# Optimization experiments

Hardware: AMD Instinct MI355X
Metric: run time of the kernel (lower is better)

## Reference

```python
import jax, jax.numpy as jnp
import numpy as np

B, S, E, H = 4, 2048, 1024, 16
HD = E // H  # per-head dim = 64


def setup_inputs() -> dict:
    key = jax.random.key(0)
    ks = jax.random.split(key, 12)
    scale = 1.0 / np.sqrt(E)
    inp = {
        "q": jax.random.normal(ks[0], (B, S, E), jnp.float32),
        "k": jax.random.normal(ks[1], (B, S, E), jnp.float32),
        "v": jax.random.normal(ks[2], (B, S, E), jnp.float32),
        # causal mask: True = masked out (matches torch masked_fill_ semantics)
        "mask": jnp.triu(jnp.ones((S, S), jnp.bool_), k=1)[None, None, :, :],
        "Wq": jax.random.normal(ks[3], (E, E), jnp.float32) * scale,
        "bq": jnp.zeros((E,), jnp.float32),
        "Wk": jax.random.normal(ks[4], (E, E), jnp.float32) * scale,
        "bk": jnp.zeros((E,), jnp.float32),
        "Wv": jax.random.normal(ks[5], (E, E), jnp.float32) * scale,
        "bv": jnp.zeros((E,), jnp.float32),
        "Wo": jax.random.normal(ks[6], (E, E), jnp.float32) * scale,
        "bo": jnp.zeros((E,), jnp.float32),
    }
    return inp


def reference(q, k, v, mask, Wq, bq, Wk, bk, Wv, bv, Wo, bo):
    # QKV projections (nn.Linear: x @ W.T + b)
    query = q @ Wq.T + bq
    key_ = k @ Wk.T + bk
    value = v @ Wv.T + bv
    # split heads: [B, S, E] -> [B, H, S, HD]
    mq = query.reshape(B, S, H, HD).transpose(0, 2, 1, 3)
    mk = key_.reshape(B, S, H, HD).transpose(0, 2, 1, 3)
    mv = value.reshape(B, S, H, HD).transpose(0, 2, 1, 3)
    # scaled dot-product attention with explicit score matrix [B, H, S, S]
    scores = jnp.einsum("bhqd,bhkd->bhqk", mq, mk) / jnp.sqrt(jnp.float32(HD))
    scores = jnp.where(mask, -jnp.inf, scores)
    probs = jax.nn.softmax(scores, axis=-1)
    ctx = jnp.einsum("bhqk,bhkd->bhqd", probs, mv)
    # merge heads and output projection
    ctx = ctx.transpose(0, 2, 1, 3).reshape(B, S, E)
    return ctx @ Wo.T + bo
```

## Files before the change

### kernel.cpp

```cpp
#include <hip/hip_runtime.h>
#include <hip/hip_bf16.h>
#include <math.h>

#define B_ 4
#define S_ 2048
#define E_ 1024
#define H_ 16
#define HD_ 64
#define NEG_ (-1e30f)
#define SC2_ 0.18033688f
#define EXP2(x) __builtin_amdgcn_exp2f(x)

typedef __bf16 bf16x8 __attribute__((ext_vector_type(8)));
typedef __bf16 bf16x4 __attribute__((ext_vector_type(4)));
typedef float f32x4 __attribute__((ext_vector_type(4)));

#define MFMA(a, b, c) __builtin_amdgcn_mfma_f32_16x16x32_bf16((a), (b), (c), 0, 0, 0)

#define GLDS16(gp, lp)                                                        \
  __builtin_amdgcn_global_load_lds(                                           \
      (const __attribute__((address_space(1))) void*)(gp),                    \
      (__attribute__((address_space(3))) void*)(lp), 16, 0, 0)

__device__ __forceinline__ bf16x8 cvt8(const float4 a, const float4 b) {
  bf16x8 r;
  r[0] = (__bf16)a.x; r[1] = (__bf16)a.y; r[2] = (__bf16)a.z; r[3] = (__bf16)a.w;
  r[4] = (__bf16)b.x; r[5] = (__bf16)b.y; r[6] = (__bf16)b.z; r[7] = (__bf16)b.w;
  return r;
}

__device__ __forceinline__ f32x4 vmax4(f32x4 a, f32x4 b) {
  f32x4 r;
  r[0] = fmaxf(a[0], b[0]); r[1] = fmaxf(a[1], b[1]);
  r[2] = fmaxf(a[2], b[2]); r[3] = fmaxf(a[3], b[3]);
  return r;
}

__global__ __launch_bounds__(256)
void cvt_all_kernel(const float* __restrict__ q, const float* __restrict__ k,
                    const float* __restrict__ v,
                    const float* __restrict__ wq, const float* __restrict__ wk,
                    const float* __restrict__ wv, const float* __restrict__ wo,
                    __bf16* __restrict__ q16, __bf16* __restrict__ k16,
                    __bf16* __restrict__ v16,
                    __bf16* __restrict__ wqb, __bf16* __restrict__ wkb,
                    __bf16* __restrict__ wvb, __bf16* __restrict__ wob)
{
  const int bx = blockIdx.x;
  const float* src;
  __bf16* dst;
  size_t off;
  if (bx < 12288) {
    const int z = bx >> 12, r = bx & 4095;
    src = (z == 0) ? q : (z == 1) ? k : v;
    dst = (z == 0) ? q16 : (z == 1) ? k16 : v16;
    off = (size_t)r * 2048 + threadIdx.x * 8;
  } else {
    const int z = (bx - 12288) >> 9, r = (bx - 12288) & 511;
    src = (z == 0) ? wq : (z == 1) ? wk : (z == 2) ? wv : wo;
    dst = (z == 0) ? wqb : (z == 1) ? wkb : (z == 2) ? wvb : wob;
    off = (size_t)r * 2048 + threadIdx.x * 8;
  }
  const float4 a = *(const float4*)&src[off];
  const float4 b = *(const float4*)&src[off + 4];
  *(bf16x8*)&dst[off] = cvt8(a, b);
}

__global__ __launch_bounds__(256)
void cvt_w_kernel(const float* __restrict__ wq, const float* __restrict__ wk,
                  const float* __restrict__ wv, const float* __restrict__ wo,
                  __bf16* __restrict__ wqb, __bf16* __restrict__ wkb,
                  __bf16* __restrict__ wvb, __bf16* __restrict__ wob)
{
  const int y = blockIdx.y;
  const float* src = (y == 0) ? wq : (y == 1) ? wk : (y == 2) ? wv : wo;
  __bf16* dst      = (y == 0) ? wqb: (y == 1) ? wkb: (y == 2) ? wvb: wob;
  const size_t i = ((size_t)blockIdx.x * 256 + threadIdx.x) * 8;
  const float4 a = *(const float4*)&src[i];
  const float4 b = *(const float4*)&src[i + 4];
  *(bf16x8*)&dst[i] = cvt8(a, b);
}

__global__ __launch_bounds__(256)
void cvt_in_kernel(const float* __restrict__ src, __bf16* __restrict__ dst)
{
  const size_t i = ((size_t)blockIdx.x * 256 + threadIdx.x) * 8;
  const float4 a = *(const float4*)&src[i];
  const float4 b = *(const float4*)&src[i + 4];
  *(bf16x8*)&dst[i] = cvt8(a, b);
}

__global__ __launch_bounds__(256, 3)
void qkv_gemm(const __bf16* __restrict__ Aq, const __bf16* __restrict__ Ak,
              const __bf16* __restrict__ Av,
              const __bf16* __restrict__ Wqb, const __bf16* __restrict__ Wkb,
              const __bf16* __restrict__ Wvb,
              const float* __restrict__ bq, const float* __restrict__ bk,
              const float* __restrict__ bv,
              __bf16* __restrict__ Qo, __bf16* __restrict__ Ko,
              __bf16* __restrict__ Vo, int zbase)
{
  __shared__ __align__(16) __bf16 sAB[2][128 * 64];
  __bf16* const sA = sAB[0];
  __bf16* const sB = sAB[1];
  const int z = (int)blockIdx.z + zbase;
  const __bf16* A   = (z == 0) ? Aq  : (z == 1) ? Ak  : Av;
  const __bf16* W   = (z == 0) ? Wqb : (z == 1) ? Wkb : Wvb;
  const float* bias = (z == 0) ? bq  : (z == 1) ? bk  : bv;

  const int t = threadIdx.x;
  const int lane = t & 63, ln = lane & 15, qd = lane >> 4;
  const int l7 = ln & 7;
  const int wv_ = t >> 6, wm = (wv_ >> 1) * 64, wn = (wv_ & 1) * 64;
  const int m0 = ((int)blockIdx.x * 8 + ((int)blockIdx.y >> 3)) * 128;
  const int n0 = ((int)blockIdx.y & 7) * 128;

  f32x4 acc[4][4] = {};
  for (int kk = 0; kk < E_; kk += 64) {
    __syncthreads();
    for (int p = 0; p < 4; ++p) {
      const int c = t + 256 * p;
      const int row = c >> 3, kc = c & 7;
      const int gcol = ((kc ^ (row & 7)) * 8);
      GLDS16(A + (size_t)(m0 + row) * E_ + kk + gcol, sA + c * 8);
      GLDS16(W + (size_t)(n0 + row) * E_ + kk + gcol, sB + c * 8);
    }
    __syncthreads();
    for (int kb2 = 0; kb2 < 2; ++kb2) {
      const int sw = ((kb2 * 4 + qd) ^ l7) * 8;
      bf16x8 af[4], bf_[4];
      for (int i = 0; i < 4; ++i)
        af[i]  = *(const bf16x8*)&sA[(wm + i * 16 + ln) * 64 + sw];
      for (int j = 0; j < 4; ++j)
        bf_[j] = *(const bf16x8*)&sB[(wn + j * 16 + ln) * 64 + sw];
      for (int i = 0; i < 4; ++i)
        for (int j = 0; j < 4; ++j)
          acc[i][j] = MFMA(af[i], bf_[j], acc[i][j]);
    }
  }

  if (z < 2) {
    __bf16* outp = (z == 0) ? Qo : Ko;
    for (int j = 0; j < 4; ++j) {
      const int n = n0 + wn + j * 16 + ln;
      const float bb = bias[n];
      const int hh = n >> 6, d = n & 63;
      for (int i = 0; i < 4; ++i) {
        for (int r2 = 0; r2 < 4; ++r2) {
          const int m = m0 + wm + i * 16 + qd * 4 + r2;
          const int b = m >> 11, s2 = m & 2047;
          float val = acc[i][j][r2] + bb;
          if (z == 0) val *= SC2_;
          outp[((size_t)(b * H_ + hh) * S_ + s2) * HD_ + d] = (__bf16)val;
        }
      }
    }
  } else {
    __syncthreads();
    __bf16* const sT = &sAB[0][0];
    for (int j = 0; j < 4; ++j) {
      const int nl = wn + j * 16 + ln;
      const float bb = bias[n0 + nl];
      const int rsw = (nl & 7) << 3;
      for (int i = 0; i < 4; ++i)
        for (int r2 = 0; r2 < 4; ++r2) {
          const int ml = wm + i * 16 + qd * 4 + r2;
          sT[nl * 128 + (ml ^ rsw)] = (__bf16)(acc[i][j][r2] + bb);
        }
    }
    __syncthreads();
    const int r = t >> 1, half = t & 1;
    const int n = n0 + r, hh = n >> 6, d = n & 63;
    const int b = m0 >> 11, s0 = m0 & 2047;
    __bf16* dstp = Vo + ((size_t)(b * H_ + hh) * HD_ + d) * S_ + s0 + half * 64;
    const int rsw = (r & 7) << 3;
    for (int c8 = 0; c8 < 8; ++c8) {
      const int mc = half * 64 + c8 * 8;
      bf16x8 vv = *(const bf16x8*)&sT[r * 128 + (mc ^ rsw)];
      *(bf16x8*)&dstp[c8 * 8] = vv;
    }
  }
}

__global__ __launch_bounds__(256, 3)
void attn_kernel(const __bf16* __restrict__ Qg, const __bf16* __restrict__ Kg,
                 const __bf16* __restrict__ Vg, __bf16* __restrict__ Og)
{
  const int slice = blockIdx.x;
  const int h = slice & 15, b = slice >> 4;
  const int qx = 31 - (int)blockIdx.y;
  const int t = threadIdx.x;
  const int wq = t >> 6;
  const int lane = t & 63;
  const int ln = lane & 15, qd = lane >> 4;
  const int l7 = ln & 7;
  const int q0 = qx * 64;
  const size_t bh = (size_t)(b * H_ + h);

  __shared__ __align__(16) __bf16 sK[128 * 64];
  __shared__ __align__(16) __bf16 sVt[64 * 128];
  __shared__ __align__(16) __bf16 sP[64 * 136];

  bf16x8 aq[2];
  {
    const __bf16* qrowp = Qg + (bh * S_ + q0 + wq * 16 + ln) * HD_;
    aq[0] = *(const bf16x8*)&qrowp[qd * 8];
    aq[1] = *(const bf16x8*)&qrowp[32 + qd * 8];
  }

  const int myq = q0 + wq * 16 + ln;

  f32x4 o[4] = {};
  float m_prev = NEG_, l_run = 0.f;

  const int ktmax = (q0 + 63) >> 7;
  for (int kt = 0; kt <= ktmax; ++kt) {
    const int k0 = kt * 128;
    __syncthreads();
    {
      const __bf16* kbase = Kg + (bh * S_ + k0) * HD_;
      const __bf16* vbase = Vg + bh * HD_ * S_ + k0;
      for (int p = 0; p < 4; ++p) {
        const int c = t + 256 * p;
        const int kr = c >> 3, kkc = c & 7;
        GLDS16(kbase + (size_t)kr * HD_ + ((kkc ^ (kr & 7)) * 8), sK + c * 8);
        const int vr = c >> 4, vkc = c & 15;
        GLDS16(vbase + (size_t)vr * S_ + ((vkc ^ (vr & 15)) * 8), sVt + c * 8);
      }
    }
    __syncthreads();

    f32x4 sc[8] = {};
    for (int kb2 = 0; kb2 < 2; ++kb2) {
      const int sw = ((kb2 * 4 + qd) ^ l7) * 8;
      for (int nt = 0; nt < 8; ++nt) {
        bf16x8 ak8 = *(const bf16x8*)&sK[(nt * 16 + ln) * 64 + sw];
        sc[nt] = MFMA(ak8, aq[kb2], sc[nt]);
      }
    }

    if (k0 + 127 > q0) {
      const int kb = k0 + qd * 4 - myq;
      for (int nt = 0; nt < 8; ++nt)
        for (int r2 = 0; r2 < 4; ++r2)
          if (kb + nt * 16 + r2 > 0) sc[nt][r2] = NEG_;
    }

    f32x4 t0 = vmax4(vmax4(sc[0], sc[1]), vmax4(sc[2], sc[3]));
    f32x4 t1 = vmax4(vmax4(sc[4], sc[5]), vmax4(sc[6], sc[7]));
    f32x4 t2 = vmax4(t0, t1);
    float mloc = fmaxf(fmaxf(t2[0], t2[1]), fmaxf(t2[2], t2[3]));
    mloc = fmaxf(mloc, __shfl_xor(mloc, 16, 64));
    mloc = fmaxf(mloc, __shfl_xor(mloc, 32, 64));

    if (!__all(mloc - m_prev <= 8.0f)) {
      const float m_new = fmaxf(m_prev, mloc);
      const float alpha = EXP2(m_prev - m_new);
      m_prev = m_new;
      l_run *= alpha;
      float af[4];
      for (int r2 = 0; r2 < 4; ++r2)
        af[r2] = __shfl(alpha, qd * 4 + r2, 64);
      for (int dt = 0; dt < 4; ++dt)
        for (int r2 = 0; r2 < 4; ++r2)
          o[dt][r2] *= af[r2];
    }

    float rsum = 0.f;
    {
      const int pb = (wq * 16 + ln) * 136 + qd * 4;
      for (int nt = 0; nt < 8; ++nt) {
        const float p0 = EXP2(sc[nt][0] - m_prev);
        const float p1 = EXP2(sc[nt][1] - m_prev);
        const float p2 = EXP2(sc[nt][2] - m_prev);
        const float p3 = EXP2(sc[nt][3] - m_prev);
        rsum += (p0 + p1) + (p2 + p3);
        bf16x4 pk;
        pk[0] = (__bf16)p0; pk[1] = (__bf16)p1;
        pk[2] = (__bf16)p2; pk[3] = (__bf16)p3;
        *(bf16x4*)&sP[pb + nt * 16] = pk;
      }
    }
    rsum += __shfl_xor(rsum, 16, 64);
    rsum += __shfl_xor(rsum, 32, 64);
    l_run += rsum;

    for (int ks = 0; ks < 4; ++ks) {
      bf16x8 ap = *(const bf16x8*)&sP[(wq * 16 + ln) * 136 + ks * 32 + qd * 8];
      const int swv = ((ks * 4 + qd) ^ ln) * 8;
      for (int dt = 0; dt < 4; ++dt) {
        bf16x8 bv8 = *(const bf16x8*)&sVt[(dt * 16 + ln) * 128 + swv];
        o[dt] = MFMA(ap, bv8, o[dt]);
      }
    }
  }

  const float linv = 1.0f / l_run;
  float inv[4];
  for (int r2 = 0; r2 < 4; ++r2)
    inv[r2] = __shfl(linv, qd * 4 + r2, 64);
  for (int r2 = 0; r2 < 4; ++r2) {
    const int qrow = q0 + wq * 16 + qd * 4 + r2;
    for (int dt = 0; dt < 4; ++dt) {
      const int d = dt * 16 + ln;
      Og[((size_t)(b * S_ + qrow)) * E_ + h * HD_ + d] = (__bf16)(o[dt][r2] * inv[r2]);
    }
  }
}

__global__ __launch_bounds__(256, 3)
void out_gemm(const __bf16* __restrict__ A, const __bf16* __restrict__ W,
              const float* __restrict__ bias, float* __restrict__ out)
{
  __shared__ __align__(16) __bf16 sA[128 * 64];
  __shared__ __align__(16) __bf16 sB[128 * 64];
  const int t = threadIdx.x;
  const int lane = t & 63, ln = lane & 15, qd = lane >> 4;
  const int l7 = ln & 7;
  const int wv_ = t >> 6, wm = (wv_ >> 1) * 64, wn = (wv_ & 1) * 64;
  const int m0 = blockIdx.y * 128, n0 = blockIdx.x * 128;

  f32x4 acc[4][4] = {};
  for (int kk = 0; kk < E_; kk += 64) {
    __syncthreads();
    for (int p = 0; p < 4; ++p) {
      const int c = t + 256 * p;
      const int row = c >> 3, kc = c & 7;
      const int gcol = ((kc ^ (row & 7)) * 8);
      GLDS16(A + (size_t)(m0 + row) * E_ + kk + gcol, sA + c * 8);
      GLDS16(W + (size_t)(n0 + row) * E_ + kk + gcol, sB + c * 8);
    }
    __syncthreads();
    for (int kb2 = 0; kb2 < 2; ++kb2) {
      const int sw = ((kb2 * 4 + qd) ^ l7) * 8;
      bf16x8 af[4], bf_[4];
      for (int i = 0; i < 4; ++i)
        af[i]  = *(const bf16x8*)&sA[(wm + i * 16 + ln) * 64 + sw];
      for (int j = 0; j < 4; ++j)
        bf_[j] = *(const bf16x8*)&sB[(wn + j * 16 + ln) * 64 + sw];
      for (int i = 0; i < 4; ++i)
        for (int j = 0; j < 4; ++j)
          acc[i][j] = MFMA(af[i], bf_[j], acc[i][j]);
    }
  }

  for (int j = 0; j < 4; ++j) {
    const int n = n0 + wn + j * 16 + ln;
    const float bb = bias[n];
    for (int i = 0; i < 4; ++i)
      for (int r2 = 0; r2 < 4; ++r2) {
        const int m = m0 + wm + i * 16 + qd * 4 + r2;
        out[(size_t)m * E_ + n] = acc[i][j][r2] + bb;
      }
  }
}

extern "C" void kernel_launch(void* const* d_in, const int* in_sizes, int n_in,
                              void* d_out, int out_size, void* d_ws, size_t ws_size,
                              hipStream_t stream)
{
  const float* q  = (const float*)d_in[0];
  const float* k  = (const float*)d_in[1];
  const float* v  = (const float*)d_in[2];
  const float* Wq = (const float*)d_in[4];
  const float* bq = (const float*)d_in[5];
  const float* Wk = (const float*)d_in[6];
  const float* bk = (const float*)d_in[7];
  const float* Wv = (const float*)d_in[8];
  const float* bv = (const float*)d_in[9];
  const float* Wo = (const float*)d_in[10];
  const float* bo = (const float*)d_in[11];
  float* out = (float*)d_out;

  const size_t NE = (size_t)B_ * S_ * E_;
  const size_t NW = (size_t)E_ * E_;
  __bf16* Wqb = (__bf16*)d_ws;
  __bf16* Wkb = Wqb + NW;
  __bf16* Wvb = Wkb + NW;
  __bf16* Wob = Wvb + NW;
  __bf16* Qb  = Wob + NW;
  __bf16* Kb  = Qb + NE;
  __bf16* Vb  = Kb + NE;

  dim3 blk(256);
  const size_t need_fat = (4 * NW + 6 * NE) * sizeof(__bf16);
  if (ws_size >= need_fat) {
    __bf16* q16 = Vb + NE;
    __bf16* k16 = q16 + NE;
    __bf16* v16 = k16 + NE;
    __bf16* Cb  = q16;
    cvt_all_kernel<<<dim3(14336), blk, 0, stream>>>(q, k, v, Wq, Wk, Wv, Wo,
                                                    q16, k16, v16,
                                                    Wqb, Wkb, Wvb, Wob);
    qkv_gemm<<<dim3(8, 64, 3), blk, 0, stream>>>(q16, k16, v16,
                                                 Wqb, Wkb, Wvb,
                                                 bq, bk, bv, Qb, Kb, Vb, 0);
    attn_kernel<<<dim3(64, 32), blk, 0, stream>>>(Qb, Kb, Vb, Cb);
    out_gemm<<<dim3(8, 64), blk, 0, stream>>>(Cb, Wob, bo, out);
  } else {
    cvt_w_kernel<<<dim3(512, 4), blk, 0, stream>>>(Wq, Wk, Wv, Wo,
                                                   Wqb, Wkb, Wvb, Wob);
    __bf16* X16 = Vb + NE;
    __bf16* Cb  = X16;
    const float* srcs[3] = {q, k, v};
    for (int z = 0; z < 3; ++z) {
      cvt_in_kernel<<<dim3(4096), blk, 0, stream>>>(srcs[z], X16);
      qkv_gemm<<<dim3(8, 64, 1), blk, 0, stream>>>(X16, X16, X16,
                                                   Wqb, Wkb, Wvb,
                                                   bq, bk, bv, Qb, Kb, Vb, z);
    }
    attn_kernel<<<dim3(64, 32), blk, 0, stream>>>(Qb, Kb, Vb, Cb);
    out_gemm<<<dim3(8, 64), blk, 0, stream>>>(Cb, Wob, bo, out);
  }
}
```

Baseline: 325.9 us.

## Switch attention kernel to 32x32 MFMA with 128-row query tiles

The attention kernel now gives each wave 32 query rows and uses 32x32x16 bf16 MFMA instead of 16x16x32, with the query tile per block grown to 128 rows and the key tile shrunk to 64. Each K/V tile loaded into LDS is reused by more query rows, fewer blocks are launched, and waves whose rows are fully masked skip the tile. The costs are a larger register footprint for the 16-element accumulators, fewer blocks in the grid, and a different causal-masking and LDS swizzle layout.

```diff
diff --git a/kernel.cpp b/kernel.cpp
--- a/kernel.cpp
+++ b/kernel.cpp
@@ -14,8 +14,10 @@
 typedef __bf16 bf16x8 __attribute__((ext_vector_type(8)));
 typedef __bf16 bf16x4 __attribute__((ext_vector_type(4)));
 typedef float f32x4 __attribute__((ext_vector_type(4)));
+typedef float f32x16 __attribute__((ext_vector_type(16)));
 
 #define MFMA(a, b, c) __builtin_amdgcn_mfma_f32_16x16x32_bf16((a), (b), (c), 0, 0, 0)
+#define MFMA32(a, b, c) __builtin_amdgcn_mfma_f32_32x32x16_bf16((a), (b), (c), 0, 0, 0)
 
 #define GLDS16(gp, lp)                                                        \
   __builtin_amdgcn_global_load_lds(                                           \
@@ -26,13 +28,6 @@
   bf16x8 r;
   r[0] = (__bf16)a.x; r[1] = (__bf16)a.y; r[2] = (__bf16)a.z; r[3] = (__bf16)a.w;
   r[4] = (__bf16)b.x; r[5] = (__bf16)b.y; r[6] = (__bf16)b.z; r[7] = (__bf16)b.w;
-  return r;
-}
-
-__device__ __forceinline__ f32x4 vmax4(f32x4 a, f32x4 b) {
-  f32x4 r;
-  r[0] = fmaxf(a[0], b[0]); r[1] = fmaxf(a[1], b[1]);
-  r[2] = fmaxf(a[2], b[2]); r[3] = fmaxf(a[3], b[3]);
   return r;
 }
 
@@ -188,69 +183,71 @@
 {
   const int slice = blockIdx.x;
   const int h = slice & 15, b = slice >> 4;
-  const int qx = 31 - (int)blockIdx.y;
+  const int qx = 15 - (int)blockIdx.y;
   const int t = threadIdx.x;
   const int wq = t >> 6;
   const int lane = t & 63;
-  const int ln = lane & 15, qd = lane >> 4;
-  const int l7 = ln & 7;
-  const int q0 = qx * 64;
+  const int r31 = lane & 31, hi = lane >> 5;
+  const int q0 = qx * 128;
   const size_t bh = (size_t)(b * H_ + h);
 
-  __shared__ __align__(16) __bf16 sK[128 * 64];
-  __shared__ __align__(16) __bf16 sVt[64 * 128];
-  __shared__ __align__(16) __bf16 sP[64 * 136];
-
-  bf16x8 aq[2];
+  __shared__ __align__(16) __bf16 sK[64 * 64];
+  __shared__ __align__(16) __bf16 sVt[64 * 64];
+  __shared__ __align__(16) __bf16 sP[128 * 72];
+
+  bf16x8 aq[4];
   {
-    const __bf16* qrowp = Qg + (bh * S_ + q0 + wq * 16 + ln) * HD_;
-    aq[0] = *(const bf16x8*)&qrowp[qd * 8];
-    aq[1] = *(const bf16x8*)&qrowp[32 + qd * 8];
-  }
-
-  const int myq = q0 + wq * 16 + ln;
-
-  f32x4 o[4] = {};
+    const __bf16* qrowp = Qg + (bh * S_ + q0 + wq * 32 + r31) * HD_;
+    for (int kb = 0; kb < 4; ++kb)
+      aq[kb] = *(const bf16x8*)&qrowp[kb * 16 + hi * 8];
+  }
+
+  const int myq = q0 + wq * 32 + r31;
+  const int prow = (wq * 32 + r31) * 72;
+
+  f32x16 o[2] = {};
   float m_prev = NEG_, l_run = 0.f;
 
-  const int ktmax = (q0 + 63) >> 7;
+  const int ktmax = (q0 + 127) >> 6;
   for (int kt = 0; kt <= ktmax; ++kt) {
-    const int k0 = kt * 128;
+    const int k0 = kt * 64;
     __syncthreads();
     {
       const __bf16* kbase = Kg + (bh * S_ + k0) * HD_;
       const __bf16* vbase = Vg + bh * HD_ * S_ + k0;
-      for (int p = 0; p < 4; ++p) {
+      for (int p = 0; p < 2; ++p) {
         const int c = t + 256 * p;
-        const int kr = c >> 3, kkc = c & 7;
-        GLDS16(kbase + (size_t)kr * HD_ + ((kkc ^ (kr & 7)) * 8), sK + c * 8);
-        const int vr = c >> 4, vkc = c & 15;
-        GLDS16(vbase + (size_t)vr * S_ + ((vkc ^ (vr & 15)) * 8), sVt + c * 8);
-      }
-    }
-    __syncthreads();
-
-    f32x4 sc[8] = {};
-    for (int kb2 = 0; kb2 < 2; ++kb2) {
-      const int sw = ((kb2 * 4 + qd) ^ l7) * 8;
-      for (int nt = 0; nt < 8; ++nt) {
-        bf16x8 ak8 = *(const bf16x8*)&sK[(nt * 16 + ln) * 64 + sw];
-        sc[nt] = MFMA(ak8, aq[kb2], sc[nt]);
-      }
-    }
-
-    if (k0 + 127 > q0) {
-      const int kb = k0 + qd * 4 - myq;
-      for (int nt = 0; nt < 8; ++nt)
-        for (int r2 = 0; r2 < 4; ++r2)
-          if (kb + nt * 16 + r2 > 0) sc[nt][r2] = NEG_;
-    }
-
-    f32x4 t0 = vmax4(vmax4(sc[0], sc[1]), vmax4(sc[2], sc[3]));
-    f32x4 t1 = vmax4(vmax4(sc[4], sc[5]), vmax4(sc[6], sc[7]));
-    f32x4 t2 = vmax4(t0, t1);
-    float mloc = fmaxf(fmaxf(t2[0], t2[1]), fmaxf(t2[2], t2[3]));
-    mloc = fmaxf(mloc, __shfl_xor(mloc, 16, 64));
+        const int row = c >> 3, kc = c & 7;
+        const int gcol = (kc ^ (row & 7)) * 8;
+        GLDS16(kbase + (size_t)row * HD_ + gcol, sK + c * 8);
+        GLDS16(vbase + (size_t)row * S_ + gcol, sVt + c * 8);
+      }
+    }
+    __syncthreads();
+
+    if (k0 > q0 + wq * 32 + 31) continue;
+
+    f32x16 sc[2] = {};
+    for (int kb = 0; kb < 4; ++kb) {
+      for (int nt = 0; nt < 2; ++nt) {
+        const int row = nt * 32 + r31;
+        const int ch = (kb * 2 + hi) ^ (row & 7);
+        bf16x8 ak8 = *(const bf16x8*)&sK[row * 64 + ch * 8];
+        sc[nt] = MFMA32(ak8, aq[kb], sc[nt]);
+      }
+    }
+
+    if (k0 + 63 > q0 + wq * 32) {
+      for (int nt = 0; nt < 2; ++nt)
+        for (int reg = 0; reg < 16; ++reg) {
+          const int kidx = k0 + nt * 32 + (reg & 3) + 8 * (reg >> 2) + 4 * hi;
+          if (kidx > myq) sc[nt][reg] = NEG_;
+        }
+    }
+
+    float mloc = sc[0][0];
+    for (int reg = 1; reg < 16; ++reg) mloc = fmaxf(mloc, sc[0][reg]);
+    for (int reg = 0; reg < 16; ++reg) mloc = fmaxf(mloc, sc[1][reg]);
     mloc = fmaxf(mloc, __shfl_xor(mloc, 32, 64));
 
     if (!__all(mloc - m_prev <= 8.0f)) {
@@ -258,52 +255,50 @@
       const float alpha = EXP2(m_prev - m_new);
       m_prev = m_new;
       l_run *= alpha;
-      float af[4];
-      for (int r2 = 0; r2 < 4; ++r2)
-        af[r2] = __shfl(alpha, qd * 4 + r2, 64);
-      for (int dt = 0; dt < 4; ++dt)
-        for (int r2 = 0; r2 < 4; ++r2)
-          o[dt][r2] *= af[r2];
+      for (int reg = 0; reg < 16; ++reg) {
+        const int ql = (reg & 3) + 8 * (reg >> 2) + 4 * hi;
+        const float ar = __shfl(alpha, ql, 64);
+        o[0][reg] *= ar;
+        o[1][reg] *= ar;
+      }
     }
 
     float rsum = 0.f;
-    {
-      const int pb = (wq * 16 + ln) * 136 + qd * 4;
-      for (int nt = 0; nt < 8; ++nt) {
-        const float p0 = EXP2(sc[nt][0] - m_prev);
-        const float p1 = EXP2(sc[nt][1] - m_prev);
-        const float p2 = EXP2(sc[nt][2] - m_prev);
-        const float p3 = EXP2(sc[nt][3] - m_prev);
+    for (int nt = 0; nt < 2; ++nt) {
+      for (int g = 0; g < 4; ++g) {
+        const float p0 = EXP2(sc[nt][4 * g + 0] - m_prev);
+        const float p1 = EXP2(sc[nt][4 * g + 1] - m_prev);
+        const float p2 = EXP2(sc[nt][4 * g + 2] - m_prev);
+        const float p3 = EXP2(sc[nt][4 * g + 3] - m_prev);
         rsum += (p0 + p1) + (p2 + p3);
         bf16x4 pk;
         pk[0] = (__bf16)p0; pk[1] = (__bf16)p1;
         pk[2] = (__bf16)p2; pk[3] = (__bf16)p3;
-        *(bf16x4*)&sP[pb + nt * 16] = pk;
-      }
-    }
-    rsum += __shfl_xor(rsum, 16, 64);
+        *(bf16x4*)&sP[prow + nt * 32 + g * 8 + hi * 4] = pk;
+      }
+    }
     rsum += __shfl_xor(rsum, 32, 64);
     l_run += rsum;
 
     for (int ks = 0; ks < 4; ++ks) {
-      bf16x8 ap = *(const bf16x8*)&sP[(wq * 16 + ln) * 136 + ks * 32 + qd * 8];
-      const int swv = ((ks * 4 + qd) ^ ln) * 8;
-      for (int dt = 0; dt < 4; ++dt) {
-        bf16x8 bv8 = *(const bf16x8*)&sVt[(dt * 16 + ln) * 128 + swv];
-        o[dt] = MFMA(ap, bv8, o[dt]);
+      bf16x8 ap = *(const bf16x8*)&sP[prow + ks * 16 + hi * 8];
+      for (int dt = 0; dt < 2; ++dt) {
+        const int row = dt * 32 + r31;
+        const int ch = (ks * 2 + hi) ^ (row & 7);
+        bf16x8 bv8 = *(const bf16x8*)&sVt[row * 64 + ch * 8];
+        o[dt] = MFMA32(ap, bv8, o[dt]);
       }
     }
   }
 
   const float linv = 1.0f / l_run;
-  float inv[4];
-  for (int r2 = 0; r2 < 4; ++r2)
-    inv[r2] = __shfl(linv, qd * 4 + r2, 64);
-  for (int r2 = 0; r2 < 4; ++r2) {
-    const int qrow = q0 + wq * 16 + qd * 4 + r2;
-    for (int dt = 0; dt < 4; ++dt) {
-      const int d = dt * 16 + ln;
-      Og[((size_t)(b * S_ + qrow)) * E_ + h * HD_ + d] = (__bf16)(o[dt][r2] * inv[r2]);
+  for (int reg = 0; reg < 16; ++reg) {
+    const int ql = (reg & 3) + 8 * (reg >> 2) + 4 * hi;
+    const float inv = __shfl(linv, ql, 64);
+    const int qrow = q0 + wq * 32 + ql;
+    for (int dt = 0; dt < 2; ++dt) {
+      const int d = dt * 32 + r31;
+      Og[((size_t)(b * S_ + qrow)) * E_ + h * HD_ + d] = (__bf16)(o[dt][reg] * inv);
     }
   }
 }
@@ -395,7 +390,7 @@
     qkv_gemm<<<dim3(8, 64, 3), blk, 0, stream>>>(q16, k16, v16,
                                                  Wqb, Wkb, Wvb,
                                                  bq, bk, bv, Qb, Kb, Vb, 0);
-    attn_kernel<<<dim3(64, 32), blk, 0, stream>>>(Qb, Kb, Vb, Cb);
+    attn_kernel<<<dim3(64, 16), blk, 0, stream>>>(Qb, Kb, Vb, Cb);
     out_gemm<<<dim3(8, 64), blk, 0, stream>>>(Cb, Wob, bo, out);
   } else {
     cvt_w_kernel<<<dim3(512, 4), blk, 0, stream>>>(Wq, Wk, Wv, Wo,
@@ -409,7 +404,7 @@
                                                    Wqb, Wkb, Wvb,
                                                    bq, bk, bv, Qb, Kb, Vb, z);
     }
-    attn_kernel<<<dim3(64, 32), blk, 0, stream>>>(Qb, Kb, Vb, Cb);
+    attn_kernel<<<dim3(64, 16), blk, 0, stream>>>(Qb, Kb, Vb, Cb);
     out_gemm<<<dim3(8, 64), blk, 0, stream>>>(Cb, Wob, bo, out);
   }
 }
```

Measured after the change: 315.9 us. 3.1% less time.
